# Performance work log

Measured on AMD Instinct MI355X. Metric: run time of the kernel, lower is better.

## Reference

```python
import jax, jax.numpy as jnp
import numpy as np

B, S, H = 2, 2048, 4096          # batch, seq_len, hidden_size
NH, NKV, D = 32, 8, 128          # query heads, kv heads (GQA), head_dim
WINDOW = 1024                    # sliding window size
EPS = 1e-5
THETA = 10000.0


def setup_inputs() -> dict:
    key = jax.random.key(0)
    ks = jax.random.split(key, 5)
    w = lambda k, shape: jax.random.normal(k, shape, jnp.float32) * 0.02
    return {
        "hidden_states": jax.random.normal(ks[0], (B, S, H), jnp.float32),
        "wq": w(ks[1], (H, NH * D)),
        "wk": w(ks[2], (H, NKV * D)),
        "wv": w(ks[3], (H, NKV * D)),
        "wo": w(ks[4], (NH * D, H)),
        "q_norm_w": jnp.ones((D,), jnp.float32),
        "k_norm_w": jnp.ones((D,), jnp.float32),
    }


def _rmsnorm(x, w):
    # Exaone4RMSNorm over the last (head_dim) axis
    var = jnp.mean(jnp.square(x.astype(jnp.float32)), axis=-1, keepdims=True)
    return (x * jax.lax.rsqrt(var + EPS)).astype(x.dtype) * w


def _rotate_half(x):
    x1, x2 = jnp.split(x, 2, axis=-1)
    return jnp.concatenate([-x2, x1], axis=-1)


def reference(hidden_states, wq, wk, wv, wo, q_norm_w, k_norm_w):
    # QKV projections (no bias)
    q = (hidden_states @ wq).reshape(B, S, NH, D)
    k = (hidden_states @ wk).reshape(B, S, NKV, D)
    v = (hidden_states @ wv).reshape(B, S, NKV, D)
    # per-head QK RMSNorm, then [B, h, S, D] layout
    q = _rmsnorm(q, q_norm_w).transpose(0, 2, 1, 3)
    k = _rmsnorm(k, k_norm_w).transpose(0, 2, 1, 3)
    v = v.transpose(0, 2, 1, 3)
    # RoPE (applied on sliding-window layers in EXAONE4)
    pos = jnp.arange(S)
    inv_freq = 1.0 / (THETA ** (jnp.arange(0, D, 2, dtype=jnp.float32) / D))
    freqs = pos[:, None].astype(jnp.float32) * inv_freq[None, :]   # [S, D/2]
    emb = jnp.concatenate([freqs, freqs], axis=-1)                 # [S, D]
    cos, sin = jnp.cos(emb), jnp.sin(emb)
    q = q * cos + _rotate_half(q) * sin
    k = k * cos + _rotate_half(k) * sin
    # GQA: repeat kv heads to match query heads
    k = jnp.repeat(k, NH // NKV, axis=1)
    v = jnp.repeat(v, NH // NKV, axis=1)
    # SDPA with causal sliding-window mask: q_pos - WINDOW < k_pos <= q_pos
    scores = jnp.einsum('bhqd,bhkd->bhqk', q, k) / jnp.sqrt(jnp.float32(D))
    diff = pos[:, None] - pos[None, :]
    mask = (diff >= 0) & (diff < WINDOW)
    scores = jnp.where(mask, scores, jnp.finfo(scores.dtype).min)
    probs = jax.nn.softmax(scores, axis=-1)
    out = jnp.einsum('bhqk,bhkd->bhqd', probs, v)
    out = out.transpose(0, 2, 1, 3).reshape(B, S, NH * D)
    return out @ wo
```

## Files before the change

### kernel.cpp

```cpp
#include <hip/hip_runtime.h>
#include <hip/hip_bf16.h>

#define B_ 2
#define S_ 2048
#define H_ 4096
#define NH_ 32
#define NKV_ 8
#define D_ 128
#define WINDOW_ 1024
#define EPS_ 1e-5f
#define M_ (B_*S_)
#define NQKV_ ((NH_ + 2*NKV_) * D_)

typedef __attribute__((ext_vector_type(8))) __bf16 bf16x8;
typedef __attribute__((ext_vector_type(4))) float f32x4;
typedef __attribute__((ext_vector_type(16))) float f32x16;

__device__ __forceinline__ unsigned short f2bf(float f) {
  union { __hip_bfloat16 h; unsigned short us; } cv;
  cv.h = __float2bfloat16(f);
  return cv.us;
}
__device__ __forceinline__ float bf2f(unsigned short u) {
  union { __hip_bfloat16 h; unsigned short us; } cv;
  cv.us = u;
  return __bfloat162float(cv.h);
}

__device__ __forceinline__ void gload16(const unsigned short* g, unsigned short* l) {
  __builtin_amdgcn_global_load_lds(
      (const __attribute__((address_space(1))) unsigned int*)(const void*)g,
      (__attribute__((address_space(3))) unsigned int*)(void*)l, 16, 0, 0);
}

__global__ __launch_bounds__(256) void transpose_convert(
    const float* __restrict__ in, unsigned short* __restrict__ out, int K, int N) {
  __shared__ float tile[32][33];
  const int n0 = blockIdx.x * 32, k0 = blockIdx.y * 32;
  const int t = threadIdx.x;
  #pragma unroll
  for (int i = 0; i < 4; ++i) {
    int e = i * 256 + t; int r = e >> 5, c = e & 31;
    tile[r][c] = in[(size_t)(k0 + r) * N + n0 + c];
  }
  __syncthreads();
  #pragma unroll
  for (int i = 0; i < 4; ++i) {
    int e = i * 256 + t; int r = e >> 5, c = e & 31;
    out[(size_t)(n0 + r) * K + k0 + c] = f2bf(tile[c][r]);
  }
}

__global__ __launch_bounds__(256) void convert_bf16_kernel(
    const float* __restrict__ in, unsigned short* __restrict__ out, int n4) {
  int i = blockIdx.x * 256 + threadIdx.x;
  if (i >= n4) return;
  float4 v = ((const float4*)in)[i];
  ushort4 o;
  o.x = f2bf(v.x); o.y = f2bf(v.y); o.z = f2bf(v.z); o.w = f2bf(v.w);
  ((ushort4*)out)[i] = o;
}

template <bool OUT_BF16>
__global__ __launch_bounds__(512) void gemm10(
    const unsigned short* __restrict__ A, const unsigned short* __restrict__ Bt,
    void* __restrict__ Cout, int N, int K) {
  __shared__ __align__(16) unsigned short lds[2][2][16384];
  const int tid = threadIdx.x;
  const int wave = tid >> 6, lane = tid & 63;
  const int l15 = lane & 15, l16 = lane >> 4;
  const int m0 = blockIdx.y * 256, n0 = blockIdx.x * 256;
  const int wmi = wave >> 2, wni = wave & 3;

  const unsigned short* asrc[4];
  const unsigned short* bsrc[4];
  #pragma unroll
  for (int it = 0; it < 4; ++it) {
    const int d = it * 512 + tid;
    const int row = d >> 3, cis = (d & 7) ^ (row & 7);
    asrc[it] = A + (size_t)(m0 + row) * K + cis * 8;
    bsrc[it] = Bt + (size_t)(n0 + row) * K + cis * 8;
  }

  int offA[2][8], offB[2][4];
  #pragma unroll
  for (int kk = 0; kk < 2; ++kk) {
    #pragma unroll
    for (int mi = 0; mi < 8; ++mi) {
      const int row = wmi * 128 + mi * 16 + l15;
      offA[kk][mi] = row * 64 + ((kk * 4 + l16) ^ (row & 7)) * 8;
    }
    #pragma unroll
    for (int ni = 0; ni < 4; ++ni) {
      const int row = wni * 64 + ni * 16 + l15;
      offB[kk][ni] = row * 64 + ((kk * 4 + l16) ^ (row & 7)) * 8;
    }
  }

  f32x4 acc[8][4];
  #pragma unroll
  for (int mi = 0; mi < 8; ++mi)
    #pragma unroll
    for (int ni = 0; ni < 4; ++ni) acc[mi][ni] = (f32x4){0.f, 0.f, 0.f, 0.f};

#define PHASE_MFMA(MOFF)                                                     \
  asm volatile("s_waitcnt lgkmcnt(0)" ::: "memory");                         \
  __builtin_amdgcn_sched_barrier(0);                                         \
  __builtin_amdgcn_s_setprio(1);                                             \
  _Pragma("unroll") for (int i = 0; i < 4; ++i)                              \
    _Pragma("unroll") for (int j = 0; j < 4; ++j)                            \
      acc[(MOFF) + i][j] = __builtin_amdgcn_mfma_f32_16x16x32_bf16(          \
          av[i], bv[j], acc[(MOFF) + i][j], 0, 0, 0);                        \
  __builtin_amdgcn_s_setprio(0);                                             \
  __builtin_amdgcn_sched_barrier(0);

  #pragma unroll
  for (int it = 0; it < 4; ++it) {
    gload16(asrc[it], &lds[0][0][it * 4096 + wave * 512]);
    gload16(bsrc[it], &lds[0][1][it * 4096 + wave * 512]);
  }
  asm volatile("s_waitcnt vmcnt(0)" ::: "memory");
  __builtin_amdgcn_sched_barrier(0);
  __builtin_amdgcn_s_barrier();

  const int nk = K >> 6;
  for (int t = 0; t < nk; ++t) {
    const int cur = t & 1, nxt = cur ^ 1;
    const unsigned short* as = lds[cur][0];
    const unsigned short* bs = lds[cur][1];
    const bool dostg = (t + 1 < nk);
    const size_t ko = (size_t)(t + 1) * 64;
    bf16x8 av[4], bv[4];

    #pragma unroll
    for (int i = 0; i < 4; ++i) av[i] = *(const bf16x8*)&as[offA[0][i]];
    #pragma unroll
    for (int j = 0; j < 4; ++j) bv[j] = *(const bf16x8*)&bs[offB[0][j]];
    if (dostg) {
      gload16(asrc[0] + ko, &lds[nxt][0][0 * 4096 + wave * 512]);
      gload16(asrc[1] + ko, &lds[nxt][0][1 * 4096 + wave * 512]);
    }
    __builtin_amdgcn_sched_barrier(0);
    __builtin_amdgcn_s_barrier();
    PHASE_MFMA(0)
    __builtin_amdgcn_s_barrier();

    #pragma unroll
    for (int i = 0; i < 4; ++i) av[i] = *(const bf16x8*)&as[offA[0][i + 4]];
    if (dostg) {
      gload16(asrc[2] + ko, &lds[nxt][0][2 * 4096 + wave * 512]);
      gload16(asrc[3] + ko, &lds[nxt][0][3 * 4096 + wave * 512]);
    }
    __builtin_amdgcn_sched_barrier(0);
    __builtin_amdgcn_s_barrier();
    PHASE_MFMA(4)
    __builtin_amdgcn_s_barrier();

    #pragma unroll
    for (int i = 0; i < 4; ++i) av[i] = *(const bf16x8*)&as[offA[1][i]];
    #pragma unroll
    for (int j = 0; j < 4; ++j) bv[j] = *(const bf16x8*)&bs[offB[1][j]];
    if (dostg) {
      gload16(bsrc[0] + ko, &lds[nxt][1][0 * 4096 + wave * 512]);
      gload16(bsrc[1] + ko, &lds[nxt][1][1 * 4096 + wave * 512]);
    }
    __builtin_amdgcn_sched_barrier(0);
    __builtin_amdgcn_s_barrier();
    PHASE_MFMA(0)
    __builtin_amdgcn_s_barrier();

    #pragma unroll
    for (int i = 0; i < 4; ++i) av[i] = *(const bf16x8*)&as[offA[1][i + 4]];
    if (dostg) {
      gload16(bsrc[2] + ko, &lds[nxt][1][2 * 4096 + wave * 512]);
      gload16(bsrc[3] + ko, &lds[nxt][1][3 * 4096 + wave * 512]);
    }
    __builtin_amdgcn_sched_barrier(0);
    __builtin_amdgcn_s_barrier();
    PHASE_MFMA(4)
    asm volatile("s_waitcnt vmcnt(0)" ::: "memory");
    __builtin_amdgcn_sched_barrier(0);
    __builtin_amdgcn_s_barrier();
  }
#undef PHASE_MFMA

  #pragma unroll
  for (int mi = 0; mi < 8; ++mi) {
    #pragma unroll
    for (int ni = 0; ni < 4; ++ni) {
      const int col = n0 + wni * 64 + ni * 16 + l15;
      #pragma unroll
      for (int j = 0; j < 4; ++j) {
        const int row = m0 + wmi * 128 + mi * 16 + l16 * 4 + j;
        if (OUT_BF16)
          ((unsigned short*)Cout)[(size_t)row * N + col] = f2bf(acc[mi][ni][j]);
        else
          ((float*)Cout)[(size_t)row * N + col] = acc[mi][ni][j];
      }
    }
  }
}

__global__ __launch_bounds__(256) void norm_rope_kernel(
    const unsigned short* __restrict__ QKVg,
    const float* __restrict__ qw, const float* __restrict__ kw,
    unsigned short* __restrict__ Qr, unsigned short* __restrict__ Kr) {
  const int bs = blockIdx.x;
  const int b = bs >> 11, s = bs & (S_ - 1);
  const int wave = threadIdx.x >> 6, lane = threadIdx.x & 63;

  float invf = 1.0f / powf(10000.0f, (float)lane * (1.0f / 64.0f));
  float sn, cs;
  sincosf((float)s * invf, &sn, &cs);

  const unsigned short* row = QKVg + (size_t)bs * NQKV_;
  const float qwa = qw[lane], qwb = qw[lane + 64];
  const float kwa = kw[lane], kwb = kw[lane + 64];
  const float scale = 0.08838834764831845f;

  for (int h = wave; h < NH_; h += 4) {
    float x0 = bf2f(row[h * D_ + lane]);
    float x1 = bf2f(row[h * D_ + 64 + lane]);
    float ss = x0 * x0 + x1 * x1;
    #pragma unroll
    for (int o = 32; o >= 1; o >>= 1) ss += __shfl_xor(ss, o);
    float r = rsqrtf(ss * (1.0f / 128.0f) + EPS_);
    x0 *= r * qwa; x1 *= r * qwb;
    float o0 = (x0 * cs - x1 * sn) * scale;
    float o1 = (x1 * cs + x0 * sn) * scale;
    size_t off = (((size_t)b * NH_ + h) * S_ + s) * D_;
    Qr[off + lane] = f2bf(o0);
    Qr[off + 64 + lane] = f2bf(o1);
  }
  for (int h = wave; h < NKV_; h += 4) {
    float x0 = bf2f(row[NH_ * D_ + h * D_ + lane]);
    float x1 = bf2f(row[NH_ * D_ + h * D_ + 64 + lane]);
    float ss = x0 * x0 + x1 * x1;
    #pragma unroll
    for (int o = 32; o >= 1; o >>= 1) ss += __shfl_xor(ss, o);
    float r = rsqrtf(ss * (1.0f / 128.0f) + EPS_);
    x0 *= r * kwa; x1 *= r * kwb;
    float o0 = x0 * cs - x1 * sn;
    float o1 = x1 * cs + x0 * sn;
    size_t off = (((size_t)b * NKV_ + h) * S_ + s) * D_;
    Kr[off + lane] = f2bf(o0);
    Kr[off + 64 + lane] = f2bf(o1);
  }
}

__global__ __launch_bounds__(256) void vtrans_kernel(
    const unsigned short* __restrict__ QKVg, unsigned short* __restrict__ Vt) {
  __shared__ unsigned short t[64][65];
  const int s0 = blockIdx.x * 64, d0 = blockIdx.y * 64;
  const int bh = blockIdx.z;
  const int b = bh >> 3, hk = bh & 7;
  const int tid = threadIdx.x;
  #pragma unroll
  for (int i = 0; i < 16; ++i) {
    int e = i * 256 + tid; int sr = e >> 6, dc = e & 63;
    t[sr][dc] = QKVg[(size_t)(b * S_ + s0 + sr) * NQKV_ + (NH_ + NKV_) * D_ + hk * D_ + d0 + dc];
  }
  __syncthreads();
  #pragma unroll
  for (int i = 0; i < 16; ++i) {
    int e = i * 256 + tid; int dr = e >> 6, sc = e & 63;
    Vt[((size_t)bh * D_ + d0 + dr) * S_ + s0 + sc] = t[sc][dr];
  }
}

__global__ __launch_bounds__(512) void attn_kernel(
    const unsigned short* __restrict__ Qr, const unsigned short* __restrict__ Kr,
    const unsigned short* __restrict__ Vt, unsigned short* __restrict__ Out) {
  const int q0 = blockIdx.x * 256;
  const int h = blockIdx.y, b = blockIdx.z, hk = h >> 2;
  const int tid = threadIdx.x;
  const int wave = tid >> 6, lane = tid & 63;
  const int l31 = lane & 31, hi = lane >> 5;
  const int qw0 = q0 + wave * 32;
  const int qpos = qw0 + l31;

  __shared__ __align__(16) unsigned short Ks[64 * 128];
  __shared__ __align__(16) unsigned short Vs[128 * 64];

  bf16x8 qf[8];
  {
    const unsigned short* qp = Qr + (((size_t)b * NH_ + h) * S_ + qpos) * D_ + hi * 8;
    #pragma unroll
    for (int ds = 0; ds < 8; ++ds) qf[ds] = *(const bf16x8*)(qp + ds * 16);
  }

  f32x16 o[4];
  #pragma unroll
  for (int i = 0; i < 4; ++i)
    #pragma unroll
    for (int j = 0; j < 16; ++j) o[i][j] = 0.f;
  float mrun = -1e30f, lrun = 0.f;

  const size_t kbase = ((size_t)b * NKV_ + hk) * S_;
  const size_t vbase = ((size_t)b * NKV_ + hk) * D_;

  const int ktlo = (q0 > 1023) ? ((q0 - 1023) & ~63) : 0;
  const int kthi = (q0 + 255) & ~63;
  const int wlo = (qw0 > 1023) ? ((qw0 - 1023) & ~63) : 0;
  const int whi = (qw0 + 31) & ~63;

  for (int kt = ktlo; kt <= kthi; kt += 64) {
    __syncthreads();
    #pragma unroll
    for (int it = 0; it < 2; ++it) {
      const int cb = it * 512 + wave * 64;
      const int c = cb + lane;
      const int rk = c >> 4, sk = c & 15;
      gload16(Kr + (kbase + kt + rk) * D_ + ((sk ^ (rk & 7)) * 8), Ks + (size_t)cb * 8);
      const int rv = c >> 3, sv = c & 7;
      gload16(Vt + (vbase + rv) * S_ + kt + ((sv ^ (rv & 7)) * 8), Vs + (size_t)cb * 8);
    }
    __syncthreads();
    if (kt < wlo || kt > whi) continue;

    f32x16 s0, s1;
    #pragma unroll
    for (int j = 0; j < 16; ++j) { s0[j] = 0.f; s1[j] = 0.f; }
    __builtin_amdgcn_s_setprio(1);
    #pragma unroll
    for (int ds = 0; ds < 8; ++ds) {
      const int g = ((ds * 2 + hi) ^ (l31 & 7)) * 8;
      bf16x8 k0 = *(const bf16x8*)&Ks[l31 * 128 + g];
      bf16x8 k1 = *(const bf16x8*)&Ks[(l31 + 32) * 128 + g];
      s0 = __builtin_amdgcn_mfma_f32_32x32x16_bf16(k0, qf[ds], s0, 0, 0, 0);
      s1 = __builtin_amdgcn_mfma_f32_32x32x16_bf16(k1, qf[ds], s1, 0, 0, 0);
    }
    __builtin_amdgcn_s_setprio(0);

    const bool fullValid = (kt + 63 <= qw0) && (kt >= qw0 - 992);
    if (!fullValid) {
      const int d0 = qpos - kt;
      #pragma unroll
      for (int r = 0; r < 16; ++r) {
        const int koff = (r & 3) + 8 * (r >> 2) + 4 * hi;
        if ((unsigned)(d0 - koff) >= (unsigned)WINDOW_) s0[r] = -1e30f;
        if ((unsigned)(d0 - koff - 32) >= (unsigned)WINDOW_) s1[r] = -1e30f;
      }
    }

    float pm = -1e30f;
    #pragma unroll
    for (int r = 0; r < 16; ++r) pm = fmaxf(pm, fmaxf(s0[r], s1[r]));
    pm = fmaxf(pm, __shfl_xor(pm, 32));
    if (!__all(pm - mrun <= 8.f)) {
      const float mnew = fmaxf(mrun, pm);
      const float scl = __expf(mrun - mnew);
      mrun = mnew;
      lrun *= scl;
      #pragma unroll
      for (int i = 0; i < 4; ++i)
        #pragma unroll
        for (int j = 0; j < 16; ++j) o[i][j] *= scl;
    }
    float ts = 0.f;
    #pragma unroll
    for (int r = 0; r < 16; ++r) {
      s0[r] = __expf(s0[r] - mrun); ts += s0[r];
      s1[r] = __expf(s1[r] - mrun); ts += s1[r];
    }
    ts += __shfl_xor(ts, 32);
    lrun += ts;

    unsigned pw[2][2][4];
    #pragma unroll
    for (int t2 = 0; t2 < 2; ++t2) {
      const f32x16 sv = t2 ? s1 : s0;
      #pragma unroll
      for (int sub = 0; sub < 2; ++sub) {
        const int bs4 = sub * 8;
        unsigned A0 = ((unsigned)f2bf(sv[bs4 + 1]) << 16) | f2bf(sv[bs4 + 0]);
        unsigned A1 = ((unsigned)f2bf(sv[bs4 + 3]) << 16) | f2bf(sv[bs4 + 2]);
        unsigned B0 = ((unsigned)f2bf(sv[bs4 + 5]) << 16) | f2bf(sv[bs4 + 4]);
        unsigned B1 = ((unsigned)f2bf(sv[bs4 + 7]) << 16) | f2bf(sv[bs4 + 6]);
        unsigned sA0 = __shfl_xor(A0, 32), sA1 = __shfl_xor(A1, 32);
        unsigned sB0 = __shfl_xor(B0, 32), sB1 = __shfl_xor(B1, 32);
        pw[t2][sub][0] = hi ? sB0 : A0;
        pw[t2][sub][1] = hi ? sB1 : A1;
        pw[t2][sub][2] = hi ? B0 : sA0;
        pw[t2][sub][3] = hi ? B1 : sA1;
      }
    }

    __builtin_amdgcn_s_setprio(1);
    #pragma unroll
    for (int t2 = 0; t2 < 2; ++t2)
      #pragma unroll
      for (int sub = 0; sub < 2; ++sub) {
        union { unsigned u[4]; bf16x8 v; } pb;
        pb.u[0] = pw[t2][sub][0]; pb.u[1] = pw[t2][sub][1];
        pb.u[2] = pw[t2][sub][2]; pb.u[3] = pw[t2][sub][3];
        #pragma unroll
        for (int dt = 0; dt < 4; ++dt) {
          const int rr = dt * 32 + l31;
          const int g = ((t2 * 4 + sub * 2 + hi) ^ (rr & 7)) * 8;
          bf16x8 vf = *(const bf16x8*)&Vs[rr * 64 + g];
          o[dt] = __builtin_amdgcn_mfma_f32_32x32x16_bf16(vf, pb.v, o[dt], 0, 0, 0);
        }
      }
    __builtin_amdgcn_s_setprio(0);
  }

  const float inv = 1.0f / lrun;
  unsigned short* op = Out + (size_t)(b * S_ + qpos) * (NH_ * D_) + h * D_;
  #pragma unroll
  for (int dt = 0; dt < 4; ++dt)
    #pragma unroll
    for (int g = 0; g < 4; ++g) {
      const int r = g * 4;
      uint2 val;
      val.x = ((unsigned)f2bf(o[dt][r + 1] * inv) << 16) | f2bf(o[dt][r + 0] * inv);
      val.y = ((unsigned)f2bf(o[dt][r + 3] * inv) << 16) | f2bf(o[dt][r + 2] * inv);
      *(uint2*)(op + dt * 32 + 8 * g + 4 * hi) = val;
    }
}

extern "C" void kernel_launch(void* const* d_in, const int* in_sizes, int n_in,
                              void* d_out, int out_size, void* d_ws, size_t ws_size,
                              hipStream_t stream) {
  const float* hidden = (const float*)d_in[0];
  const float* wq = (const float*)d_in[1];
  const float* wk = (const float*)d_in[2];
  const float* wv = (const float*)d_in[3];
  const float* wo = (const float*)d_in[4];
  const float* qw = (const float*)d_in[5];
  const float* kw = (const float*)d_in[6];
  float* out = (float*)d_out;

  char* ws = (char*)d_ws;
  unsigned short* wqkv = (unsigned short*)(ws);
  unsigned short* kr   = (unsigned short*)(ws);
  unsigned short* vt   = (unsigned short*)(ws + ((size_t)8 << 20));
  unsigned short* attn = (unsigned short*)(ws + ((size_t)16 << 20));
  unsigned short* qkvg = (unsigned short*)(ws + ((size_t)48 << 20));
  unsigned short* wot  = (unsigned short*)(ws + ((size_t)48 << 20));
  unsigned short* hb   = (unsigned short*)d_out;
  unsigned short* qr   = (unsigned short*)d_out + ((size_t)16 << 20);

  transpose_convert<<<dim3(NH_ * D_ / 32, H_ / 32), 256, 0, stream>>>(wq, wqkv, H_, NH_ * D_);
  transpose_convert<<<dim3(NKV_ * D_ / 32, H_ / 32), 256, 0, stream>>>(
      wk, wqkv + (size_t)NH_ * D_ * H_, H_, NKV_ * D_);
  transpose_convert<<<dim3(NKV_ * D_ / 32, H_ / 32), 256, 0, stream>>>(
      wv, wqkv + (size_t)(NH_ + NKV_) * D_ * H_, H_, NKV_ * D_);

  convert_bf16_kernel<<<(M_ * H_ / 4 + 255) / 256, 256, 0, stream>>>(hidden, hb, M_ * H_ / 4);

  gemm10<true><<<dim3(NQKV_ / 256, M_ / 256), 512, 0, stream>>>(hb, wqkv, qkvg, NQKV_, H_);

  norm_rope_kernel<<<M_, 256, 0, stream>>>(qkvg, qw, kw, qr, kr);

  vtrans_kernel<<<dim3(S_ / 64, D_ / 64, B_ * NKV_), 256, 0, stream>>>(qkvg, vt);

  transpose_convert<<<dim3(H_ / 32, H_ / 32), 256, 0, stream>>>(wo, wot, NH_ * D_, H_);

  attn_kernel<<<dim3(S_ / 256, NH_, B_), 512, 0, stream>>>(qr, kr, vt, attn);

  gemm10<false><<<dim3(H_ / 256, M_ / 256), 512, 0, stream>>>(attn, wot, out, H_, H_);
}
```

Before: 545.9 us.

## Add BK=32 GEMM variant with smaller LDS for QKV and vectorize weight transpose

Adds gemm11, a 256x256-tile GEMM that steps K by 32 instead of 64. This halves the LDS footprint and raises the launch-bounds occupancy hint to 4, trading more barriers per K for more resident waves. The QKV projection now uses gemm11, while the output projection keeps gemm10. The weight transpose-convert kernel now uses 64x64 tiles with float4 loads, converts to bf16 before the LDS stage, and writes ushort4 stores, cutting memory transactions on the weight preprocessing.

```diff
diff --git a/kernel.cpp b/kernel.cpp
--- a/kernel.cpp
+++ b/kernel.cpp
@@ -35,19 +35,27 @@
 
 __global__ __launch_bounds__(256) void transpose_convert(
     const float* __restrict__ in, unsigned short* __restrict__ out, int K, int N) {
-  __shared__ float tile[32][33];
-  const int n0 = blockIdx.x * 32, k0 = blockIdx.y * 32;
-  const int t = threadIdx.x;
+  __shared__ unsigned short t[64][72];
+  const int n0 = blockIdx.x * 64, k0 = blockIdx.y * 64;
+  const int tid = threadIdx.x;
+  const int rr = tid >> 4, cc = (tid & 15) * 4;
   #pragma unroll
   for (int i = 0; i < 4; ++i) {
-    int e = i * 256 + t; int r = e >> 5, c = e & 31;
-    tile[r][c] = in[(size_t)(k0 + r) * N + n0 + c];
+    const int r = i * 16 + rr;
+    float4 v = *(const float4*)&in[(size_t)(k0 + r) * N + n0 + cc];
+    t[cc + 0][r] = f2bf(v.x);
+    t[cc + 1][r] = f2bf(v.y);
+    t[cc + 2][r] = f2bf(v.z);
+    t[cc + 3][r] = f2bf(v.w);
   }
   __syncthreads();
   #pragma unroll
   for (int i = 0; i < 4; ++i) {
-    int e = i * 256 + t; int r = e >> 5, c = e & 31;
-    out[(size_t)(n0 + r) * K + k0 + c] = f2bf(tile[c][r]);
+    const int r = i * 16 + rr;
+    ushort4 o;
+    o.x = t[r][cc + 0]; o.y = t[r][cc + 1];
+    o.z = t[r][cc + 2]; o.w = t[r][cc + 3];
+    *(ushort4*)&out[(size_t)(n0 + r) * K + k0 + cc] = o;
   }
 }
 
@@ -59,6 +67,116 @@
   ushort4 o;
   o.x = f2bf(v.x); o.y = f2bf(v.y); o.z = f2bf(v.z); o.w = f2bf(v.w);
   ((ushort4*)out)[i] = o;
+}
+
+template <bool OUT_BF16>
+__global__ __launch_bounds__(512, 4) void gemm11(
+    const unsigned short* __restrict__ A, const unsigned short* __restrict__ Bt,
+    void* __restrict__ Cout, int N, int K) {
+  __shared__ __align__(16) unsigned short lds[2][2][8192];
+  const int tid = threadIdx.x;
+  const int wave = tid >> 6, lane = tid & 63;
+  const int l15 = lane & 15, l16 = lane >> 4;
+  const int m0 = blockIdx.y * 256, n0 = blockIdx.x * 256;
+  const int wmi = wave >> 2, wni = wave & 3;
+
+  const unsigned short* asrc[2];
+  const unsigned short* bsrc[2];
+  #pragma unroll
+  for (int it = 0; it < 2; ++it) {
+    const int d = it * 512 + tid;
+    const int r2 = d >> 3, cl = d & 7;
+    const int cu = cl ^ (r2 & 7);
+    const int grow = 2 * r2 + (cu >> 2);
+    const int gk = (cu & 3) * 8;
+    asrc[it] = A + (size_t)(m0 + grow) * K + gk;
+    bsrc[it] = Bt + (size_t)(n0 + grow) * K + gk;
+  }
+
+  int offA[8], offB[4];
+  #pragma unroll
+  for (int mi = 0; mi < 8; ++mi) {
+    const int row = wmi * 128 + mi * 16 + l15;
+    const int r2 = row >> 1, cl = (row & 1) * 4 + l16;
+    offA[mi] = r2 * 64 + (cl ^ (r2 & 7)) * 8;
+  }
+  #pragma unroll
+  for (int ni = 0; ni < 4; ++ni) {
+    const int row = wni * 64 + ni * 16 + l15;
+    const int r2 = row >> 1, cl = (row & 1) * 4 + l16;
+    offB[ni] = r2 * 64 + (cl ^ (r2 & 7)) * 8;
+  }
+
+  f32x4 acc[8][4];
+  #pragma unroll
+  for (int mi = 0; mi < 8; ++mi)
+    #pragma unroll
+    for (int ni = 0; ni < 4; ++ni) acc[mi][ni] = (f32x4){0.f, 0.f, 0.f, 0.f};
+
+#define STG(buf, kt)                                                         \
+  { _Pragma("unroll") for (int it = 0; it < 2; ++it) {                       \
+      const int dst = it * 4096 + wave * 512;                                \
+      gload16(asrc[it] + (size_t)(kt) * 32, &lds[buf][0][dst]);              \
+      gload16(bsrc[it] + (size_t)(kt) * 32, &lds[buf][1][dst]);              \
+    } }
+
+#define PHASE_MFMA(MOFF)                                                     \
+  asm volatile("s_waitcnt lgkmcnt(0)" ::: "memory");                         \
+  __builtin_amdgcn_sched_barrier(0);                                         \
+  __builtin_amdgcn_s_setprio(1);                                             \
+  _Pragma("unroll") for (int i = 0; i < 4; ++i)                              \
+    _Pragma("unroll") for (int j = 0; j < 4; ++j)                            \
+      acc[(MOFF) + i][j] = __builtin_amdgcn_mfma_f32_16x16x32_bf16(          \
+          av[i], bv[j], acc[(MOFF) + i][j], 0, 0, 0);                        \
+  __builtin_amdgcn_s_setprio(0);                                             \
+  __builtin_amdgcn_sched_barrier(0);
+
+  const int nk = K >> 5;
+  STG(0, 0)
+  for (int t = 0; t < nk; ++t) {
+    const int cur = t & 1;
+    if (t + 1 < nk) {
+      STG(cur ^ 1, t + 1)
+      asm volatile("s_waitcnt vmcnt(4)" ::: "memory");
+    } else {
+      asm volatile("s_waitcnt vmcnt(0)" ::: "memory");
+    }
+    __builtin_amdgcn_sched_barrier(0);
+    __builtin_amdgcn_s_barrier();
+    __builtin_amdgcn_sched_barrier(0);
+    const unsigned short* as = lds[cur][0];
+    const unsigned short* bs = lds[cur][1];
+    bf16x8 av[4], bv[4];
+    #pragma unroll
+    for (int i = 0; i < 4; ++i) av[i] = *(const bf16x8*)&as[offA[i]];
+    #pragma unroll
+    for (int j = 0; j < 4; ++j) bv[j] = *(const bf16x8*)&bs[offB[j]];
+    PHASE_MFMA(0)
+    __builtin_amdgcn_s_barrier();
+    #pragma unroll
+    for (int i = 0; i < 4; ++i) av[i] = *(const bf16x8*)&as[offA[i + 4]];
+    PHASE_MFMA(4)
+    __builtin_amdgcn_s_barrier();
+    __builtin_amdgcn_sched_barrier(0);
+  }
+#undef STG
+#undef PHASE_MFMA
+
+  #pragma unroll
+  for (int mi = 0; mi < 8; ++mi) {
+    #pragma unroll
+    for (int ni = 0; ni < 4; ++ni) {
+      const int col = n0 + wni * 64 + ni * 16 + l15;
+      #pragma unroll
+      for (int j = 0; j < 4; ++j) {
+        const int row = m0 + wmi * 128 + mi * 16 + l16 * 4 + j;
+        if (OUT_BF16)
+          ((unsigned short*)Cout)[(size_t)row * N + col] = f2bf(acc[mi][ni][j]);
+        else
+          ((float*)Cout)[(size_t)row * N + col] = acc[mi][ni][j];
+      }
+    }
+  }
 }
 
 template <bool OUT_BF16>
@@ -441,21 +559,21 @@
   unsigned short* hb   = (unsigned short*)d_out;
   unsigned short* qr   = (unsigned short*)d_out + ((size_t)16 << 20);
 
-  transpose_convert<<<dim3(NH_ * D_ / 32, H_ / 32), 256, 0, stream>>>(wq, wqkv, H_, NH_ * D_);
-  transpose_convert<<<dim3(NKV_ * D_ / 32, H_ / 32), 256, 0, stream>>>(
+  transpose_convert<<<dim3(NH_ * D_ / 64, H_ / 64), 256, 0, stream>>>(wq, wqkv, H_, NH_ * D_);
+  transpose_convert<<<dim3(NKV_ * D_ / 64, H_ / 64), 256, 0, stream>>>(
       wk, wqkv + (size_t)NH_ * D_ * H_, H_, NKV_ * D_);
-  transpose_convert<<<dim3(NKV_ * D_ / 32, H_ / 32), 256, 0, stream>>>(
+  transpose_convert<<<dim3(NKV_ * D_ / 64, H_ / 64), 256, 0, stream>>>(
       wv, wqkv + (size_t)(NH_ + NKV_) * D_ * H_, H_, NKV_ * D_);
 
   convert_bf16_kernel<<<(M_ * H_ / 4 + 255) / 256, 256, 0, stream>>>(hidden, hb, M_ * H_ / 4);
 
-  gemm10<true><<<dim3(NQKV_ / 256, M_ / 256), 512, 0, stream>>>(hb, wqkv, qkvg, NQKV_, H_);
+  gemm11<true><<<dim3(NQKV_ / 256, M_ / 256), 512, 0, stream>>>(hb, wqkv, qkvg, NQKV_, H_);
 
   norm_rope_kernel<<<M_, 256, 0, stream>>>(qkvg, qw, kw, qr, kr);
 
   vtrans_kernel<<<dim3(S_ / 64, D_ / 64, B_ * NKV_), 256, 0, stream>>>(qkvg, vt);
 
-  transpose_convert<<<dim3(H_ / 32, H_ / 32), 256, 0, stream>>>(wo, wot, NH_ * D_, H_);
+  transpose_convert<<<dim3(H_ / 64, H_ / 64), 256, 0, stream>>>(wo, wot, NH_ * D_, H_);
 
   attn_kernel<<<dim3(S_ / 256, NH_, B_), 512, 0, stream>>>(qr, kr, vt, attn);
 
```

Result: slower. 1.826 ms (+234.5%).
